# Optimization experiments

Hardware: AMD Instinct MI355X
Metric: run time of the kernel (lower is better)

The kernel has to match this reference:

```python
import jax, jax.numpy as jnp
import numpy as np

WS = 6        # window size -> N = 36 tokens per window
HEADS = 16

def _rel_index(ws):
    coords = np.stack(np.meshgrid(np.arange(ws), np.arange(ws), indexing='ij')).reshape(2, -1)
    rel = coords[:, :, None] - coords[:, None, :] + (ws - 1)
    return jnp.asarray(rel[0] * (2 * ws - 1) + rel[1])  # (N, N) int

REL_IDX = _rel_index(WS)

def _ln(x, g, b, eps=1e-5):
    m = x.mean(-1, keepdims=True)
    v = x.var(-1, keepdims=True)
    return (x - m) / jnp.sqrt(v + eps) * g + b

def setup_inputs() -> dict:
    key = jax.random.key(0)
    ks = jax.random.split(key, 6)
    B, H, W, C = 16, 96, 96, 512
    hid = 4 * C
    s = 0.02
    return {
        'x': jax.random.normal(ks[0], (B, H, W, C), jnp.float32),
        'w_qkv': jax.random.normal(ks[1], (C, 3 * C), jnp.float32) * s,
        'w_proj': jax.random.normal(ks[2], (C, C), jnp.float32) * s,
        'b_proj': jnp.zeros((C,), jnp.float32),
        'rel_bias': jax.random.normal(ks[3], ((2 * WS - 1) ** 2, HEADS), jnp.float32) * s,
        'ln1_g': jnp.ones((C,), jnp.float32), 'ln1_b': jnp.zeros((C,), jnp.float32),
        'ln2_g': jnp.ones((C,), jnp.float32), 'ln2_b': jnp.zeros((C,), jnp.float32),
        'w_fc1': jax.random.normal(ks[4], (C, hid), jnp.float32) * s,
        'b_fc1': jnp.zeros((hid,), jnp.float32),
        'w_fc2': jax.random.normal(ks[5], (hid, C), jnp.float32) * s,
        'b_fc2': jnp.zeros((C,), jnp.float32),
    }

def reference(x, w_qkv, w_proj, b_proj, rel_bias, ln1_g, ln1_b, ln2_g, ln2_b, w_fc1, b_fc1, w_fc2, b_fc2):
    B, H, W, C = x.shape
    h, d, N = HEADS, C // HEADS, WS * WS
    nh, nw = H // WS, W // WS
    # window partition: (B,H,W,C) -> (B*nh*nw, N, C)
    xw = x.reshape(B, nh, WS, nw, WS, C).transpose(0, 1, 3, 2, 4, 5).reshape(B * nh * nw, N, C)
    xn = _ln(xw, ln1_g, ln1_b)
    qkv = xn @ w_qkv
    q, k, v = jnp.split(qkv, 3, axis=-1)
    to_heads = lambda t: t.reshape(-1, N, h, d).transpose(0, 2, 1, 3)  # (B_, h, N, d)
    q = to_heads(q) * (d ** -0.5)
    k = to_heads(k)
    v = to_heads(v)
    attn = jnp.einsum('bhnd,bhmd->bhnm', q, k)
    bias = rel_bias[REL_IDX.reshape(-1)].reshape(N, N, h).transpose(2, 0, 1)  # (h, N, N)
    attn = jax.nn.softmax(attn + bias[None], axis=-1)
    o = jnp.einsum('bhnm,bhmd->bhnd', attn, v).transpose(0, 2, 1, 3).reshape(-1, N, C)
    o = o @ w_proj + b_proj
    # un-window; NOTE: source has no residual around attention (x is replaced)
    x2 = o.reshape(B, nh, nw, WS, WS, C).transpose(0, 1, 3, 2, 4, 5).reshape(B, H, W, C)
    xm = _ln(x2, ln2_g, ln2_b)
    mlp = jax.nn.gelu(xm @ w_fc1 + b_fc1, approximate=False) @ w_fc2 + b_fc2
    return x2 + mlp
```

## Files before the change

### kernel.cpp

```cpp
#include <hip/hip_runtime.h>
#include <stdint.h>

#define TOK 147456
#define CCH 512

typedef __attribute__((ext_vector_type(8))) short short8;
typedef __attribute__((ext_vector_type(4))) float f32x4;

struct alignas(8) US4 { unsigned short a, b, c, d; };

typedef __attribute__((address_space(3))) void lds_void;
typedef const __attribute__((address_space(1))) void gbl_void;

__device__ inline void gload16(const void* g, void* l) {
    __builtin_amdgcn_global_load_lds((gbl_void*)g, (lds_void*)l, 16, 0, 0);
}

__device__ inline unsigned short f2bf(float f) {
    union { float f; unsigned u; } v{f};
    unsigned r = v.u + 0x7fffu + ((v.u >> 16) & 1u);
    return (unsigned short)(r >> 16);
}
__device__ inline float bf2f(unsigned short h) {
    union { unsigned u; float f; } v; v.u = ((unsigned)h) << 16; return v.f;
}

__global__ void wprep(const float* __restrict__ in, unsigned short* __restrict__ out,
                      int K, int N) {
    int idx = blockIdx.x * 256 + threadIdx.x;
    if (idx >= K * N) return;
    int k = idx / N, n = idx % N;
    out[(size_t)n * K + k] = f2bf(in[idx]);
}

__global__ void biasprep(const float* __restrict__ rb, float* __restrict__ bb) {
    int idx = blockIdx.x * 256 + threadIdx.x;
    if (idx >= 16 * 48 * 48) return;
    int h = idx / 2304, rem = idx % 2304, r = rem / 48, c = rem % 48;
    float v = -1e9f;
    if (r < 36 && c < 36) {
        int dy = r / 6 - c / 6 + 5;
        int dx = r % 6 - c % 6 + 5;
        v = rb[(dy * 11 + dx) * 16 + h];
    }
    bb[idx] = v;
}

__global__ __launch_bounds__(256) void ln_k(const float* __restrict__ x,
                                            const float* __restrict__ g,
                                            const float* __restrict__ b,
                                            unsigned short* __restrict__ out, int ntok) {
    int lane = threadIdx.x & 63;
    int tok = blockIdx.x * 4 + (threadIdx.x >> 6);
    if (tok >= ntok) return;
    const float4* xr = (const float4*)(x + (size_t)tok * CCH);
    float4 v0 = xr[lane], v1 = xr[lane + 64];
    float s  = v0.x + v0.y + v0.z + v0.w + v1.x + v1.y + v1.z + v1.w;
    float s2 = v0.x*v0.x + v0.y*v0.y + v0.z*v0.z + v0.w*v0.w
             + v1.x*v1.x + v1.y*v1.y + v1.z*v1.z + v1.w*v1.w;
#pragma unroll
    for (int off = 32; off; off >>= 1) { s += __shfl_xor(s, off); s2 += __shfl_xor(s2, off); }
    float mean = s * (1.f / 512.f);
    float var  = s2 * (1.f / 512.f) - mean * mean;
    float inv  = rsqrtf(var + 1e-5f);
    const float4* gp = (const float4*)g;
    const float4* bp = (const float4*)b;
    float4 g0 = gp[lane], g1 = gp[lane + 64], b0 = bp[lane], b1 = bp[lane + 64];
    US4 o0, o1;
    o0.a = f2bf((v0.x - mean) * inv * g0.x + b0.x);
    o0.b = f2bf((v0.y - mean) * inv * g0.y + b0.y);
    o0.c = f2bf((v0.z - mean) * inv * g0.z + b0.z);
    o0.d = f2bf((v0.w - mean) * inv * g0.w + b0.w);
    o1.a = f2bf((v1.x - mean) * inv * g1.x + b1.x);
    o1.b = f2bf((v1.y - mean) * inv * g1.y + b1.y);
    o1.c = f2bf((v1.z - mean) * inv * g1.z + b1.z);
    o1.d = f2bf((v1.w - mean) * inv * g1.w + b1.w);
    unsigned short* op = out + (size_t)tok * CCH;
    *(US4*)(op + 4 * lane)       = o0;
    *(US4*)(op + 256 + 4 * lane) = o1;
}

__global__ __launch_bounds__(256) void ln_bf(const unsigned short* __restrict__ x,
                                             const float* __restrict__ g,
                                             const float* __restrict__ b,
                                             unsigned short* __restrict__ out, int ntok) {
    int lane = threadIdx.x & 63;
    int tok = blockIdx.x * 4 + (threadIdx.x >> 6);
    if (tok >= ntok) return;
    short8 v = *(const short8*)(x + (size_t)tok * CCH + lane * 8);
    float f[8];
#pragma unroll
    for (int j = 0; j < 8; ++j) f[j] = bf2f((unsigned short)v[j]);
    float s = 0.f, s2 = 0.f;
#pragma unroll
    for (int j = 0; j < 8; ++j) { s += f[j]; s2 += f[j] * f[j]; }
#pragma unroll
    for (int off = 32; off; off >>= 1) { s += __shfl_xor(s, off); s2 += __shfl_xor(s2, off); }
    float mean = s * (1.f / 512.f);
    float var  = s2 * (1.f / 512.f) - mean * mean;
    float inv  = rsqrtf(var + 1e-5f);
    const float4* gp = (const float4*)g + lane * 2;
    const float4* bp = (const float4*)b + lane * 2;
    float4 g0 = gp[0], g1 = gp[1], b0 = bp[0], b1 = bp[1];
    float gg[8] = {g0.x, g0.y, g0.z, g0.w, g1.x, g1.y, g1.z, g1.w};
    float bb[8] = {b0.x, b0.y, b0.z, b0.w, b1.x, b1.y, b1.z, b1.w};
    short8 o;
#pragma unroll
    for (int j = 0; j < 8; ++j) o[j] = (short)f2bf((f[j] - mean) * inv * gg[j] + bb[j]);
    *(short8*)(out + (size_t)tok * CCH + lane * 8) = o;
}

__global__ __launch_bounds__(256) void attn_mfma(const unsigned short* __restrict__ qkv,
                                                 const float* __restrict__ biasb,
                                                 unsigned short* __restrict__ o) {
    __shared__ __align__(16) unsigned short p_lds[4][48 * 64];
    __shared__ __align__(16) unsigned short v_lds[4][32 * 64];

    int tid  = threadIdx.x;
    int wv   = tid >> 6;
    int lane = tid & 63;
    int l15  = lane & 15;
    int g    = lane >> 4;

    int wid = blockIdx.x * 4 + wv;
    int h   = wid & 15;
    int win = wid >> 4;
    int img  = win >> 8;
    int wrow = (win >> 4) & 15;
    int wcol = win & 15;
    int tok_base = (img * 96 + wrow * 6) * 96 + wcol * 6;

    unsigned short* pw = p_lds[wv];
    unsigned short* vw = v_lds[wv];

    #define TOKOF(r) (tok_base + (r) + 90 * ((r) / 6))

    short8 z8 = {};
    for (int e = lane; e < 224; e += 64) {
        if (e < 128) {
            int ch = e >> 2, kst = 32 + (e & 3) * 8;
            *(short8*)(vw + ch * 64 + (kst ^ ((ch & 7) << 3))) = z8;
        } else {
            int ee = e - 128; int q = ee >> 1, kst = 48 + (ee & 1) * 8;
            *(short8*)(pw + q * 64 + (kst ^ ((q & 7) << 3))) = z8;
        }
    }

    for (int e = lane; e < 144; e += 64) {
        int r = e >> 2, c0 = (e & 3) * 8;
        short8 vv = *(const short8*)(qkv + (size_t)TOKOF(r) * 1536 + 1024 + h * 32 + c0);
#pragma unroll
        for (int j = 0; j < 8; ++j) {
            int ch = c0 + j;
            vw[ch * 64 + (r ^ ((ch & 7) << 3))] = (unsigned short)vv[j];
        }
    }

    short8 qf[3], kf[3];
#pragma unroll
    for (int t = 0; t < 3; ++t) {
        int r = t * 16 + l15;
        if (r < 36) {
            size_t ba = (size_t)TOKOF(r) * 1536 + h * 32 + g * 8;
            qf[t] = *(const short8*)(qkv + ba);
            kf[t] = *(const short8*)(qkv + ba + 512);
        } else { qf[t] = z8; kf[t] = z8; }
    }

    f32x4 s[3][3] = {};
#pragma unroll
    for (int mt = 0; mt < 3; ++mt)
#pragma unroll
        for (int nt = 0; nt < 3; ++nt)
            s[mt][nt] = __builtin_amdgcn_mfma_f32_16x16x32_bf16(qf[mt], kf[nt], s[mt][nt], 0, 0, 0);

    const float SCALE = 0.17677669529663687f;
    const float* bh = biasb + h * 2304;
#pragma unroll
    for (int mt = 0; mt < 3; ++mt) {
#pragma unroll
        for (int r = 0; r < 4; ++r) {
            int row = mt * 16 + g * 4 + r;
            const float* bb = bh + row * 48 + l15;
            float v0 = fmaf(s[mt][0][r], SCALE, bb[0]);
            float v1 = fmaf(s[mt][1][r], SCALE, bb[16]);
            float v2 = fmaf(s[mt][2][r], SCALE, bb[32]);
            float m = fmaxf(fmaxf(v0, v1), v2);
#pragma unroll
            for (int off = 1; off < 16; off <<= 1) m = fmaxf(m, __shfl_xor(m, off));
            float e0 = __expf(v0 - m), e1 = __expf(v1 - m), e2 = __expf(v2 - m);
            float sm = e0 + e1 + e2;
#pragma unroll
            for (int off = 1; off < 16; off <<= 1) sm += __shfl_xor(sm, off);
            float inv = 1.f / sm;
            int sw = (row & 7) << 3;
            unsigned short* pr = pw + row * 64;
            pr[(l15)      ^ sw] = f2bf(e0 * inv);
            pr[(16 + l15) ^ sw] = f2bf(e1 * inv);
            pr[(32 + l15) ^ sw] = f2bf(e2 * inv);
        }
    }

    f32x4 oacc[3][2] = {};
#pragma unroll
    for (int ks = 0; ks < 2; ++ks) {
        int kst = ks * 32 + g * 8;
        short8 bfr[2];
#pragma unroll
        for (int nt = 0; nt < 2; ++nt) {
            int c = nt * 16 + l15;
            bfr[nt] = *(const short8*)(vw + c * 64 + (kst ^ ((c & 7) << 3)));
        }
#pragma unroll
        for (int mt = 0; mt < 3; ++mt) {
            int q = mt * 16 + l15;
            short8 pa = *(const short8*)(pw + q * 64 + (kst ^ ((q & 7) << 3)));
#pragma unroll
            for (int nt = 0; nt < 2; ++nt)
                oacc[mt][nt] = __builtin_amdgcn_mfma_f32_16x16x32_bf16(pa, bfr[nt], oacc[mt][nt], 0, 0, 0);
        }
    }

#pragma unroll
    for (int mt = 0; mt < 3; ++mt) {
#pragma unroll
        for (int r = 0; r < 4; ++r) {
            int q = mt * 16 + g * 4 + r;
            if (q < 36) {
                size_t rb = (size_t)TOKOF(q) * 512 + h * 32;
#pragma unroll
                for (int nt = 0; nt < 2; ++nt)
                    o[rb + nt * 16 + l15] = f2bf(oacc[mt][nt][r]);
            }
        }
    }
    #undef TOKOF
}

template <int EPI>
__global__ __launch_bounds__(512, 1) void gemm8(const unsigned short* __restrict__ A,
                                                const unsigned short* __restrict__ Bt,
                                                int M, int N, int K,
                                                const float* __restrict__ bias,
                                                const unsigned short* __restrict__ resid,
                                                void* __restrict__ Cout) {
    extern __shared__ char lds[];
    int tid = threadIdx.x;
    int w = tid >> 6, lane = tid & 63;
    int l15 = lane & 15, grp = lane >> 4;
    int wm = w >> 2, wn = w & 3;

    int nbn = N >> 8;
    int nwg = gridDim.x;
    int q = nwg >> 3, r = nwg & 7;
    int xcd = blockIdx.x & 7, pos_ = blockIdx.x >> 3;
    int wgid = (xcd < r ? xcd * (q + 1) : r * (q + 1) + (xcd - r) * q) + pos_;
    int bm = wgid / nbn, bn = wgid % nbn;

    int NT = K >> 5;

    int u = (tid & 7) ^ ((tid >> 3) & 7);
    int srow = ((tid >> 3) << 1) + (u >> 2);
    int scol = (u & 3) * 8;
    const unsigned short* aSrc = A  + ((size_t)bm * 256 + srow) * (size_t)K + scol;
    const unsigned short* bSrc = Bt + ((size_t)bn * 256 + srow) * (size_t)K + scol;

    #define STAGE_A(t) do { char* s_ = lds + ((t) & 3) * 32768; size_t ko_ = (size_t)(t) * 32; \
        gload16(aSrc + ko_, s_ + tid * 16); \
        gload16(aSrc + ko_ + (size_t)128 * K, s_ + 8192 + tid * 16); } while (0)
    #define STAGE_B(t) do { char* s_ = lds + ((t) & 3) * 32768 + 16384; size_t ko_ = (size_t)(t) * 32; \
        gload16(bSrc + ko_, s_ + tid * 16); \
        gload16(bSrc + ko_ + (size_t)128 * K, s_ + 8192 + tid * 16); } while (0)

    int rpos = (grp + (l15 & 1) * 4) ^ (l15 >> 1);
    int aRd = (wm * 64 + (l15 >> 1)) * 128 + rpos * 16;
    int bRd = 16384 + (wn * 32 + (l15 >> 1)) * 128 + rpos * 16;

    f32x4 acc[8][4] = {};

    STAGE_A(0); STAGE_B(0); STAGE_A(1); STAGE_B(1); STAGE_A(2); STAGE_B(2);
    asm volatile("s_waitcnt vmcnt(8)" ::: "memory");
    __builtin_amdgcn_s_barrier();

    for (int t = 0; t < NT; ++t) {
        char* sb = lds + (t & 3) * 32768;
        short8 af[4], bf[4], ag[4];

#pragma unroll
        for (int m = 0; m < 4; ++m) af[m] = *(const short8*)(sb + aRd + m * 1024);
#pragma unroll
        for (int n = 0; n < 4; ++n) bf[n] = *(const short8*)(sb + bRd + n * 1024);
        if (t + 3 < NT) STAGE_A(t + 3);
        asm volatile("s_waitcnt lgkmcnt(0)" ::: "memory");
        __builtin_amdgcn_sched_barrier(0);
        __builtin_amdgcn_s_setprio(1);
#pragma unroll
        for (int m = 0; m < 4; ++m)
#pragma unroll
            for (int n = 0; n < 4; ++n)
                acc[m][n] = __builtin_amdgcn_mfma_f32_16x16x32_bf16(af[m], bf[n], acc[m][n], 0, 0, 0);
        __builtin_amdgcn_s_setprio(0);
        __builtin_amdgcn_s_barrier();

#pragma unroll
        for (int m = 0; m < 4; ++m) ag[m] = *(const short8*)(sb + aRd + (m + 4) * 1024);
        if (t + 3 < NT) STAGE_B(t + 3);
        if (t + 1 < NT) {
            if (t + 3 < NT)      asm volatile("s_waitcnt vmcnt(8)" ::: "memory");
            else if (t + 2 < NT) asm volatile("s_waitcnt vmcnt(4)" ::: "memory");
            else                 asm volatile("s_waitcnt vmcnt(0)" ::: "memory");
        }
        asm volatile("s_waitcnt lgkmcnt(0)" ::: "memory");
        __builtin_amdgcn_sched_barrier(0);
        __builtin_amdgcn_s_setprio(1);
#pragma unroll
        for (int m = 0; m < 4; ++m)
#pragma unroll
            for (int n = 0; n < 4; ++n)
                acc[m + 4][n] = __builtin_amdgcn_mfma_f32_16x16x32_bf16(ag[m], bf[n], acc[m + 4][n], 0, 0, 0);
        __builtin_amdgcn_s_setprio(0);
        __builtin_amdgcn_s_barrier();
    }
    #undef STAGE_A
    #undef STAGE_B

    int row0 = bm * 256 + wm * 128 + grp * 4;
    int col0 = bn * 256 + wn * 64 + l15;
#pragma unroll
    for (int m = 0; m < 8; ++m) {
#pragma unroll
        for (int n = 0; n < 4; ++n) {
            int col = col0 + n * 16;
            float bv = (EPI == 0) ? 0.f : bias[col];
#pragma unroll
            for (int r2 = 0; r2 < 4; ++r2) {
                int row = row0 + m * 16 + r2;
                size_t idx = (size_t)row * N + col;
                float val = acc[m][n][r2] + bv;
                if (EPI == 0) {
                    ((unsigned short*)Cout)[idx] = f2bf(val);
                } else if (EPI == 1) {
                    ((unsigned short*)Cout)[idx] = f2bf(val);
                } else if (EPI == 2) {
                    float u3 = val * val * val;
                    float z2 = 1.5957691216f * (val + 0.044715f * u3);
                    float e = __expf(z2);
                    float th = 1.f - 2.f / (e + 1.f);
                    float ge = 0.5f * val * (1.f + th);
                    ((unsigned short*)Cout)[idx] = f2bf(ge);
                } else {
                    ((float*)Cout)[idx] = val + bf2f(resid[idx]);
                }
            }
        }
    }
}

extern "C" void kernel_launch(void* const* d_in, const int* in_sizes, int n_in,
                              void* d_out, int out_size, void* d_ws, size_t ws_size,
                              hipStream_t stream) {
    const float* x       = (const float*)d_in[0];
    const float* w_qkv   = (const float*)d_in[1];
    const float* w_proj  = (const float*)d_in[2];
    const float* b_proj  = (const float*)d_in[3];
    const float* relb    = (const float*)d_in[4];
    const float* ln1g    = (const float*)d_in[5];
    const float* ln1b    = (const float*)d_in[6];
    const float* ln2g    = (const float*)d_in[7];
    const float* ln2b    = (const float*)d_in[8];
    const float* w_fc1   = (const float*)d_in[9];
    const float* b_fc1   = (const float*)d_in[10];
    const float* w_fc2   = (const float*)d_in[11];
    const float* b_fc2   = (const float*)d_in[12];
    float* out = (float*)d_out;

    hipFuncSetAttribute(reinterpret_cast<const void*>(&gemm8<0>),
                        hipFuncAttributeMaxDynamicSharedMemorySize, 131072);
    hipFuncSetAttribute(reinterpret_cast<const void*>(&gemm8<1>),
                        hipFuncAttributeMaxDynamicSharedMemorySize, 131072);
    hipFuncSetAttribute(reinterpret_cast<const void*>(&gemm8<2>),
                        hipFuncAttributeMaxDynamicSharedMemorySize, 131072);
    hipFuncSetAttribute(reinterpret_cast<const void*>(&gemm8<3>),
                        hipFuncAttributeMaxDynamicSharedMemorySize, 131072);

    char* w = (char*)d_ws;
    unsigned short* wT_qkv  = (unsigned short*)w; w += (size_t)1536 * 512 * 2;
    unsigned short* wT_proj = (unsigned short*)w; w += (size_t)512  * 512 * 2;
    unsigned short* wT_fc1  = (unsigned short*)w; w += (size_t)2048 * 512 * 2;
    unsigned short* wT_fc2  = (unsigned short*)w; w += (size_t)512  * 2048 * 2;
    float* biasb            = (float*)w;          w += (size_t)16 * 48 * 48 * 4;
    size_t wbytes = (size_t)(w - (char*)d_ws);

    int nchunk = 16;
    for (int c = 1; c <= 16; c *= 2) {
        size_t tokc = TOK / c;
        if (wbytes + tokc * 6144 <= ws_size) { nchunk = c; break; }
    }
    size_t tokc = TOK / nchunk;
    unsigned short* buf1 = (unsigned short*)w;
    unsigned short* buf2 = (unsigned short*)(w + tokc * 1024);
    unsigned short* buf3 = (unsigned short*)(w + tokc * 5120);

    wprep<<<(512 * 1536 + 255) / 256, 256, 0, stream>>>(w_qkv,  wT_qkv,  512, 1536);
    wprep<<<(512 * 512  + 255) / 256, 256, 0, stream>>>(w_proj, wT_proj, 512, 512);
    wprep<<<(512 * 2048 + 255) / 256, 256, 0, stream>>>(w_fc1,  wT_fc1,  512, 2048);
    wprep<<<(2048 * 512 + 255) / 256, 256, 0, stream>>>(w_fc2,  wT_fc2,  2048, 512);
    biasprep<<<(16 * 48 * 48 + 255) / 256, 256, 0, stream>>>(relb, biasb);

    int Mc = (int)tokc;
    int gm = Mc / 256;
    int imgs = Mc / 9216;

    for (int c = 0; c < nchunk; ++c) {
        size_t toff = (size_t)c * tokc;
        const float* xc = x + toff * CCH;
        float* outc = out + toff * CCH;

        ln_k<<<Mc / 4, 256, 0, stream>>>(xc, ln1g, ln1b, buf1, Mc);
        gemm8<0><<<gm * 6, 512, 131072, stream>>>(buf1, wT_qkv, Mc, 1536, 512,
                                                  nullptr, nullptr, buf2);
        attn_mfma<<<imgs * 1024, 256, 0, stream>>>(buf2, biasb, buf1);
        gemm8<1><<<gm * 2, 512, 131072, stream>>>(buf1, wT_proj, Mc, 512, 512,
                                                  b_proj, nullptr, buf3);
        ln_bf<<<Mc / 4, 256, 0, stream>>>(buf3, ln2g, ln2b, buf1, Mc);
        gemm8<2><<<gm * 8, 512, 131072, stream>>>(buf1, wT_fc1, Mc, 2048, 512,
                                                  b_fc1, nullptr, buf2);
        gemm8<3><<<gm * 2, 512, 131072, stream>>>(buf2, wT_fc2, Mc, 512, 2048,
                                                  b_fc2, buf3, outc);
    }
}
```

Measured before the change: 1.682 ms.

## Shrink GEMM tile to 128x256 with 3-stage pipeline for multi-block occupancy

Replaces the 256x256 GEMM tile (4-stage LDS ring, 128KB) with a 128x256 tile on a 3-stage ring of 24KB per stage, one MFMA phase per K step, and launch bounds raised to allow several blocks per CU. The goal is more resident waves and a larger grid, so latency is hidden by other blocks and wave quantisation improves. In exchange, A-tile reuse per loaded B element halves, raising global/LDS traffic per FLOP, and the prefetch distance is shorter. Launch bounds of 4 may also cap register use for 32 accumulators.

```diff
diff --git a/kernel.cpp b/kernel.cpp
--- a/kernel.cpp
+++ b/kernel.cpp
@@ -238,7 +238,7 @@
 }
 
 template <int EPI>
-__global__ __launch_bounds__(512, 1) void gemm8(const unsigned short* __restrict__ A,
+__global__ __launch_bounds__(512, 4) void gemm8(const unsigned short* __restrict__ A,
                                                 const unsigned short* __restrict__ Bt,
                                                 int M, int N, int K,
                                                 const float* __restrict__ bias,
@@ -262,35 +262,38 @@
     int u = (tid & 7) ^ ((tid >> 3) & 7);
     int srow = ((tid >> 3) << 1) + (u >> 2);
     int scol = (u & 3) * 8;
-    const unsigned short* aSrc = A  + ((size_t)bm * 256 + srow) * (size_t)K + scol;
+    const unsigned short* aSrc = A  + ((size_t)bm * 128 + srow) * (size_t)K + scol;
     const unsigned short* bSrc = Bt + ((size_t)bn * 256 + srow) * (size_t)K + scol;
 
-    #define STAGE_A(t) do { char* s_ = lds + ((t) & 3) * 32768; size_t ko_ = (size_t)(t) * 32; \
-        gload16(aSrc + ko_, s_ + tid * 16); \
-        gload16(aSrc + ko_ + (size_t)128 * K, s_ + 8192 + tid * 16); } while (0)
-    #define STAGE_B(t) do { char* s_ = lds + ((t) & 3) * 32768 + 16384; size_t ko_ = (size_t)(t) * 32; \
-        gload16(bSrc + ko_, s_ + tid * 16); \
-        gload16(bSrc + ko_ + (size_t)128 * K, s_ + 8192 + tid * 16); } while (0)
-
-    int rpos = (grp + (l15 & 1) * 4) ^ (l15 >> 1);
-    int aRd = (wm * 64 + (l15 >> 1)) * 128 + rpos * 16;
-    int bRd = 16384 + (wn * 32 + (l15 >> 1)) * 128 + rpos * 16;
-
-    f32x4 acc[8][4] = {};
-
-    STAGE_A(0); STAGE_B(0); STAGE_A(1); STAGE_B(1); STAGE_A(2); STAGE_B(2);
-    asm volatile("s_waitcnt vmcnt(8)" ::: "memory");
-    __builtin_amdgcn_s_barrier();
+    #define STAGE(t) do { char* s_ = lds + ((t) % 3) * 24576; size_t ko_ = (size_t)(t) * 32; \
+        gload16(aSrc + ko_,                   s_ + tid * 16); \
+        gload16(bSrc + ko_,                   s_ + 8192  + tid * 16); \
+        gload16(bSrc + ko_ + (size_t)128 * K, s_ + 16384 + tid * 16); } while (0)
+
+    int rpos = (grp + (l15 & 1) * 4) ^ ((l15 >> 1) & 7);
+    int aRd = (wm * 32 + (l15 >> 1)) * 128 + rpos * 16;
+    int bRd = 8192 + (wn * 32 + (l15 >> 1)) * 128 + rpos * 16;
+
+    f32x4 acc[4][4] = {};
+
+    STAGE(0); STAGE(1);
 
     for (int t = 0; t < NT; ++t) {
-        char* sb = lds + (t & 3) * 32768;
-        short8 af[4], bf[4], ag[4];
-
+        if (t + 2 < NT) {
+            STAGE(t + 2);
+            asm volatile("s_waitcnt vmcnt(6)" ::: "memory");
+        } else if (t + 1 < NT) {
+            asm volatile("s_waitcnt vmcnt(3)" ::: "memory");
+        } else {
+            asm volatile("s_waitcnt vmcnt(0)" ::: "memory");
+        }
+        __builtin_amdgcn_s_barrier();
+        char* sb = lds + (t % 3) * 24576;
+        short8 af[4], bf[4];
 #pragma unroll
         for (int m = 0; m < 4; ++m) af[m] = *(const short8*)(sb + aRd + m * 1024);
 #pragma unroll
         for (int n = 0; n < 4; ++n) bf[n] = *(const short8*)(sb + bRd + n * 1024);
-        if (t + 3 < NT) STAGE_A(t + 3);
         asm volatile("s_waitcnt lgkmcnt(0)" ::: "memory");
         __builtin_amdgcn_sched_barrier(0);
         __builtin_amdgcn_s_setprio(1);
@@ -301,33 +304,13 @@
                 acc[m][n] = __builtin_amdgcn_mfma_f32_16x16x32_bf16(af[m], bf[n], acc[m][n], 0, 0, 0);
         __builtin_amdgcn_s_setprio(0);
         __builtin_amdgcn_s_barrier();
-
-#pragma unroll
-        for (int m = 0; m < 4; ++m) ag[m] = *(const short8*)(sb + aRd + (m + 4) * 1024);
-        if (t + 3 < NT) STAGE_B(t + 3);
-        if (t + 1 < NT) {
-            if (t + 3 < NT)      asm volatile("s_waitcnt vmcnt(8)" ::: "memory");
-            else if (t + 2 < NT) asm volatile("s_waitcnt vmcnt(4)" ::: "memory");
-            else                 asm volatile("s_waitcnt vmcnt(0)" ::: "memory");
-        }
-        asm volatile("s_waitcnt lgkmcnt(0)" ::: "memory");
-        __builtin_amdgcn_sched_barrier(0);
-        __builtin_amdgcn_s_setprio(1);
-#pragma unroll
-        for (int m = 0; m < 4; ++m)
-#pragma unroll
-            for (int n = 0; n < 4; ++n)
-                acc[m + 4][n] = __builtin_amdgcn_mfma_f32_16x16x32_bf16(ag[m], bf[n], acc[m + 4][n], 0, 0, 0);
-        __builtin_amdgcn_s_setprio(0);
-        __builtin_amdgcn_s_barrier();
-    }
-    #undef STAGE_A
-    #undef STAGE_B
-
-    int row0 = bm * 256 + wm * 128 + grp * 4;
+    }
+    #undef STAGE
+
+    int row0 = bm * 128 + wm * 64 + grp * 4;
     int col0 = bn * 256 + wn * 64 + l15;
 #pragma unroll
-    for (int m = 0; m < 8; ++m) {
+    for (int m = 0; m < 4; ++m) {
 #pragma unroll
         for (int n = 0; n < 4; ++n) {
             int col = col0 + n * 16;
@@ -375,13 +358,13 @@
     float* out = (float*)d_out;
 
     hipFuncSetAttribute(reinterpret_cast<const void*>(&gemm8<0>),
-                        hipFuncAttributeMaxDynamicSharedMemorySize, 131072);
+                        hipFuncAttributeMaxDynamicSharedMemorySize, 73728);
     hipFuncSetAttribute(reinterpret_cast<const void*>(&gemm8<1>),
-                        hipFuncAttributeMaxDynamicSharedMemorySize, 131072);
+                        hipFuncAttributeMaxDynamicSharedMemorySize, 73728);
     hipFuncSetAttribute(reinterpret_cast<const void*>(&gemm8<2>),
-                        hipFuncAttributeMaxDynamicSharedMemorySize, 131072);
+                        hipFuncAttributeMaxDynamicSharedMemorySize, 73728);
     hipFuncSetAttribute(reinterpret_cast<const void*>(&gemm8<3>),
-                        hipFuncAttributeMaxDynamicSharedMemorySize, 131072);
+                        hipFuncAttributeMaxDynamicSharedMemorySize, 73728);
 
     char* w = (char*)d_ws;
     unsigned short* wT_qkv  = (unsigned short*)w; w += (size_t)1536 * 512 * 2;
@@ -408,7 +391,7 @@
     biasprep<<<(16 * 48 * 48 + 255) / 256, 256, 0, stream>>>(relb, biasb);
 
     int Mc = (int)tokc;
-    int gm = Mc / 256;
+    int gm = Mc / 128;
     int imgs = Mc / 9216;
 
     for (int c = 0; c < nchunk; ++c) {
@@ -417,15 +400,15 @@
         float* outc = out + toff * CCH;
 
         ln_k<<<Mc / 4, 256, 0, stream>>>(xc, ln1g, ln1b, buf1, Mc);
-        gemm8<0><<<gm * 6, 512, 131072, stream>>>(buf1, wT_qkv, Mc, 1536, 512,
-                                                  nullptr, nullptr, buf2);
+        gemm8<0><<<gm * 6, 512, 73728, stream>>>(buf1, wT_qkv, Mc, 1536, 512,
+                                                 nullptr, nullptr, buf2);
         attn_mfma<<<imgs * 1024, 256, 0, stream>>>(buf2, biasb, buf1);
-        gemm8<1><<<gm * 2, 512, 131072, stream>>>(buf1, wT_proj, Mc, 512, 512,
-                                                  b_proj, nullptr, buf3);
+        gemm8<1><<<gm * 2, 512, 73728, stream>>>(buf1, wT_proj, Mc, 512, 512,
+                                                 b_proj, nullptr, buf3);
         ln_bf<<<Mc / 4, 256, 0, stream>>>(buf3, ln2g, ln2b, buf1, Mc);
-        gemm8<2><<<gm * 8, 512, 131072, stream>>>(buf1, wT_fc1, Mc, 2048, 512,
-                                                  b_fc1, nullptr, buf2);
-        gemm8<3><<<gm * 2, 512, 131072, stream>>>(buf2, wT_fc2, Mc, 512, 2048,
-                                                  b_fc2, buf3, outc);
-    }
-}
+        gemm8<2><<<gm * 8, 512, 73728, stream>>>(buf1, wT_fc1, Mc, 2048, 512,
+                                                 b_fc1, nullptr, buf2);
+        gemm8<3><<<gm * 2, 512, 73728, stream>>>(buf2, wT_fc2, Mc, 512, 2048,
+                                                 b_fc2, buf3, outc);
+    }
+}
```

Result: no change. 1.662 ms (-1.1%).
